# Optimization experiments

Hardware: AMD Instinct MI355X
Metric: run time of the kernel (lower is better)

## Reference

```python
import jax, jax.numpy as jnp
import numpy as np

B, T, TC = 128, 300, 20          # batch, words per sentence, chars per word
DW, DC = 16, 32                  # word / char embedding dims
UC, UM = 32, 64                  # char-LSTM units, main-LSTM units
POS, PAR = 20, 8                 # extra feature dims
VW, VC = 1834, 132               # vocab sizes
DIN = DW + UC + POS + PAR        # 76, input dim of main BiLSTM


def setup_inputs() -> dict:
    key = jax.random.key(0)
    ks = jax.random.split(key, 16)
    s = 0.05
    f32 = jnp.float32
    return dict(
        word_in=jax.random.randint(ks[0], (B, T), 0, VW, dtype=jnp.int32),
        char_in=jax.random.randint(ks[1], (B, T, TC), 0, VC, dtype=jnp.int32),
        input_pos=jax.random.normal(ks[2], (B, T, POS), f32),
        input_par=jax.random.normal(ks[3], (B, T, PAR), f32),
        emb_wor=jax.random.normal(ks[4], (VW, DW), f32) * s,
        emb_char=jax.random.normal(ks[5], (VC, DC), f32) * s,
        char_Wx=jax.random.normal(ks[6], (DC, 4 * UC), f32) * s,
        char_Wh=jax.random.normal(ks[7], (UC, 4 * UC), f32) * s,
        char_b=jnp.zeros((4 * UC,), f32),
        fwd_Wx=jax.random.normal(ks[8], (DIN, 4 * UM), f32) * s,
        fwd_Wh=jax.random.normal(ks[9], (UM, 4 * UM), f32) * s,
        fwd_b=jnp.zeros((4 * UM,), f32),
        bwd_Wx=jax.random.normal(ks[10], (DIN, 4 * UM), f32) * s,
        bwd_Wh=jax.random.normal(ks[11], (UM, 4 * UM), f32) * s,
        bwd_b=jnp.zeros((4 * UM,), f32),
        dense_W=jax.random.normal(ks[12], (2 * UM, 4), f32) * s,
        dense_b=jnp.zeros((4,), f32),
    )


def _lstm(x, mask, Wx, Wh, b):
    """Masked Keras-style LSTM (gate order i,f,g,o). x:(N,S,D) mask:(N,S) bool.
    Masked steps carry state (Keras mask_zero semantics). Returns (N,S,U)."""
    U = Wh.shape[0]
    xz = jnp.einsum('nsd,df->nsf', x, Wx) + b  # hoist input projection out of scan

    def step(carry, inp):
        h, c = carry
        z_x, m = inp
        z = z_x + h @ Wh
        i, f, g, o = jnp.split(z, 4, axis=-1)
        c_new = jax.nn.sigmoid(f) * c + jax.nn.sigmoid(i) * jnp.tanh(g)
        h_new = jax.nn.sigmoid(o) * jnp.tanh(c_new)
        m = m[:, None]
        h = jnp.where(m, h_new, h)
        c = jnp.where(m, c_new, c)
        return (h, c), h

    N = x.shape[0]
    h0 = jnp.zeros((N, U), x.dtype)
    (_, _), hs = jax.lax.scan(step, (h0, h0),
                              (jnp.swapaxes(xz, 0, 1), jnp.swapaxes(mask, 0, 1)))
    return jnp.swapaxes(hs, 0, 1)


def reference(word_in, char_in, input_pos, input_par,
              emb_wor, emb_char, char_Wx, char_Wh, char_b,
              fwd_Wx, fwd_Wh, fwd_b, bwd_Wx, bwd_Wh, bwd_b,
              dense_W, dense_b):
    # word embeddings: (B,T,DW)
    ew = emb_wor[word_in]
    # char embeddings, TimeDistributed over words: (B*T, TC, DC)
    ec = emb_char[char_in].reshape(B * T, TC, DC)
    cmask = (char_in != 0).reshape(B * T, TC)
    # char LSTM, return_sequences=False -> final (last-valid) state
    ch = _lstm(ec, cmask, char_Wx, char_Wh, char_b)[:, -1, :].reshape(B, T, UC)
    # concat word emb, char encoding, extra features -> (B,T,DIN)
    x = jnp.concatenate([ew, ch, input_pos, input_par], axis=-1)
    wmask = word_in != 0
    hf = _lstm(x, wmask, fwd_Wx, fwd_Wh, fwd_b)
    hb = _lstm(x[:, ::-1], wmask[:, ::-1], bwd_Wx, bwd_Wh, bwd_b)[:, ::-1]
    h = jnp.concatenate([hf, hb], axis=-1)  # (B,T,2*UM)
    return jax.nn.softmax(h @ dense_W + dense_b, axis=-1)  # (B,T,4)
```

## Files before the change

kernel.cpp:

```cpp
#include <hip/hip_runtime.h>
#include <hip/hip_bf16.h>

#define B_ 128
#define T_ 300
#define TC_ 20
#define DW_ 16
#define DC_ 32
#define UC_ 32
#define UM_ 64
#define POS_ 20
#define PAR_ 8
#define VW_ 1834
#define VC_ 132
#define DIN_ 76
#define XS_ 80
#define NROW (B_*T_)

typedef _Float16 half_t;
typedef half_t h2 __attribute__((ext_vector_type(2)));

__device__ __forceinline__ float fast_sig(float x){
  return __builtin_amdgcn_rcpf(1.f + __expf(-x));
}
__device__ __forceinline__ float fast_tanh(float x){
  return __builtin_amdgcn_rcpf(1.f + __expf(-2.f*x))*2.f - 1.f;
}
__device__ __forceinline__ float dot2u(unsigned int a, unsigned int b, float acc){
  union{unsigned int u; h2 h;} x, y; x.u = a; y.u = b;
#if __has_builtin(__builtin_amdgcn_fdot2)
  return __builtin_amdgcn_fdot2(x.h, y.h, acc, false);
#else
  return acc + (float)x.h.x*(float)y.h.x + (float)x.h.y*(float)y.h.y;
#endif
}
__device__ __forceinline__ float us2f(unsigned short s){
  union{unsigned short s; half_t h;} x; x.s = s; return (float)x.h;
}

__global__ void k_xzc(const float* __restrict__ emb_char, const float* __restrict__ Wx,
                      const float* __restrict__ bias, float* __restrict__ xzc){
  int v = blockIdx.x, j = threadIdx.x;
  float acc = bias[j];
  #pragma unroll
  for (int k=0;k<DC_;k++) acc += emb_char[v*DC_+k]*Wx[k*(4*UC_)+j];
  xzc[v*(4*UC_)+j] = acc;
}

__global__ void k_chT(const float* __restrict__ Wh, half_t* __restrict__ o){
  int t = blockIdx.x*256 + threadIdx.x;
  int j = t >> 5, k = t & 31;
  o[t] = (half_t)Wh[k*(4*UC_)+j];
}

__global__ void k_whT(const float* __restrict__ Whf, const float* __restrict__ Whb,
                      half_t* __restrict__ o){
  int t = blockIdx.x*256 + threadIdx.x;
  int dir = t >> 14;
  int j = (t >> 6) & 255;
  int k = t & 63;
  const float* W = dir ? Whb : Whf;
  o[t] = (half_t)W[k*(4*UM_)+j];
}

__global__ void k_wxT(const float* __restrict__ Wxf, const float* __restrict__ Wxb,
                      half_t* __restrict__ o){
  int t = blockIdx.x*256 + threadIdx.x;
  int dir = t / (256*96);
  int r = t % (256*96);
  int jj = r / 96, k = r % 96;
  const float* W = dir ? Wxb : Wxf;
  o[t] = (k < DIN_) ? (half_t)W[k*(4*UM_)+jj] : (half_t)0.f;
}

__global__ void k_xfill(const int* __restrict__ word_in, const float* __restrict__ emb_wor,
                        const float* __restrict__ pos, const float* __restrict__ par,
                        float* __restrict__ x){
  int r = blockIdx.x*4 + threadIdx.x/80;
  int c = threadIdx.x%80;
  float v;
  if (c < DW_)                     v = emb_wor[word_in[r]*DW_ + c];
  else if (c < DW_+UC_)            return;
  else if (c < DW_+UC_+POS_)       v = pos[r*POS_ + (c-(DW_+UC_))];
  else if (c < DIN_)               v = par[r*PAR_ + (c-(DW_+UC_+POS_))];
  else                             return;
  x[r*XS_ + c] = v;
}

__global__ __launch_bounds__(512,4) void k_char(const int* __restrict__ char_in,
        const float* __restrict__ xzc, const half_t* __restrict__ chT,
        float* __restrict__ x){
  __shared__ unsigned int hbuf2[8][16];
  __shared__ float2 zex[8][64];
  __shared__ int sidx[8*TC_];
  const int tid = threadIdx.x;
  const int w8 = tid >> 6;
  const int lane = tid & 63;
  const int u = lane & 31;
  const int half = lane >> 5;
  const int seq = blockIdx.x*8 + w8;

  if (tid < 8*TC_) sidx[tid] = char_in[blockIdx.x*(8*TC_) + tid];
  if (half==0 && u<16) hbuf2[w8][u] = 0;

  unsigned int wa[16], wb[16];
  {
    const uint4* pa = reinterpret_cast<const uint4*>(chT + (half*64+u)*32);
    const uint4* pb = reinterpret_cast<const uint4*>(chT + (half*64+32+u)*32);
    #pragma unroll
    for (int q=0;q<4;q++){
      uint4 va = pa[q], vb = pb[q];
      wa[q*4+0]=va.x; wa[q*4+1]=va.y; wa[q*4+2]=va.z; wa[q*4+3]=va.w;
      wb[q*4+0]=vb.x; wb[q*4+1]=vb.y; wb[q*4+2]=vb.z; wb[q*4+3]=vb.w;
    }
  }
  #pragma unroll
  for (int k=0;k<16;k++){ asm volatile("" : "+v"(wa[k])); asm volatile("" : "+v"(wb[k])); }
  __syncthreads();

  float h = 0.f, c = 0.f;
  int idx = sidx[w8*TC_ + 0];
  float za0 = xzc[idx*(4*UC_) + half*64 + u];
  float zb0 = xzc[idx*(4*UC_) + half*64 + 32 + u];

  for (int t=0; t<TC_; t++){
    int idxn = (t+1 < TC_) ? sidx[w8*TC_ + t+1] : 0;
    float zan = xzc[idxn*(4*UC_) + half*64 + u];
    float zbn = xzc[idxn*(4*UC_) + half*64 + 32 + u];

    float za = za0, zb = zb0;
    const uint4* hb = reinterpret_cast<const uint4*>(&hbuf2[w8][0]);
    uint4 q0=hb[0], q1=hb[1], q2=hb[2], q3=hb[3];
    unsigned int hu[16] = {q0.x,q0.y,q0.z,q0.w, q1.x,q1.y,q1.z,q1.w,
                           q2.x,q2.y,q2.z,q2.w, q3.x,q3.y,q3.z,q3.w};
    #pragma unroll
    for (int k=0;k<16;k++){
      za = dot2u(wa[k], hu[k], za);
      zb = dot2u(wb[k], hu[k], zb);
    }
    zex[w8][lane] = make_float2(za, zb);
    if (half == 0){
      float2 p = zex[w8][32+u];
      float zi = za, zf = zb, zg = p.x, zo = p.y;
      float cn = fast_sig(zf)*c + fast_sig(zi)*fast_tanh(zg);
      float hn = fast_sig(zo)*fast_tanh(cn);
      bool m = (idx != 0);
      c = m ? cn : c;
      h = m ? hn : h;
      reinterpret_cast<half_t*>(&hbuf2[w8][0])[u] = (half_t)h;
    }
    idx = idxn; za0 = zan; zb0 = zbn;
  }
  if (half == 0) x[seq*XS_ + DW_ + u] = h;
}

__global__ __launch_bounds__(512,1) void k_xz(const float* __restrict__ x,
      const half_t* __restrict__ wxT_h,
      const float* __restrict__ b_f, const float* __restrict__ b_b,
      half_t* __restrict__ xz){
  __shared__ unsigned int xs[16][40];
  const int j = threadIdx.x;
  const int jj = j & 255;
  const bool bwd = (j >= 256);
  const float bj = bwd ? b_b[jj] : b_f[jj];
  const int u = jj & 63, g = jj >> 6;
  const int ocol = (bwd ? 256 : 0) + u*4 + g;

  unsigned int wq[40];
  {
    const uint4* p = reinterpret_cast<const uint4*>(wxT_h + (size_t)((bwd?256:0)+jj)*96);
    #pragma unroll
    for (int q=0;q<10;q++){
      uint4 v = p[q];
      wq[q*4+0]=v.x; wq[q*4+1]=v.y; wq[q*4+2]=v.z; wq[q*4+3]=v.w;
    }
  }
  #pragma unroll
  for (int k=0;k<40;k++) asm volatile("" : "+v"(wq[k]));

  const int rowbase = blockIdx.x*16;
  for (int i=j; i<16*40; i+=512){
    int r = i/40, q = i%40;
    unsigned int pk = 0;
    if (q < 38){
      float v0 = x[(size_t)(rowbase+r)*XS_ + 2*q];
      float v1 = x[(size_t)(rowbase+r)*XS_ + 2*q+1];
      union{h2 h; unsigned int u;} cv; cv.h = h2{(half_t)v0,(half_t)v1};
      pk = cv.u;
    }
    xs[r][q] = pk;
  }
  __syncthreads();

  for (int r=0; r<16; r++){
    const uint4* xr = reinterpret_cast<const uint4*>(&xs[r][0]);
    float acc = bj;
    #pragma unroll
    for (int q=0;q<10;q++){
      uint4 v = xr[q];
      acc = dot2u(wq[q*4+0], v.x, acc);
      acc = dot2u(wq[q*4+1], v.y, acc);
      acc = dot2u(wq[q*4+2], v.z, acc);
      acc = dot2u(wq[q*4+3], v.w, acc);
    }
    xz[(size_t)(rowbase+r)*512 + ocol] = (half_t)acc;
  }
}

__global__ __launch_bounds__(256,1) void k_rnn(const half_t* __restrict__ xz,
      const int* __restrict__ word_in, const half_t* __restrict__ whT_h,
      float* __restrict__ hcat){
  __shared__ float zpart[2][4*UM_][4];
  __shared__ unsigned int hbuf2[4][32];
  __shared__ int wm[T_];
  const int j = threadIdx.x;
  const int w = j >> 6;
  const int l = j & 63;
  const int dir = blockIdx.x & 1;
  const int b = blockIdx.x >> 1;
  const int sw = (l >> 3) & 3;

  unsigned int wt[4][8];
  {
    const half_t* wbase = whT_h + (size_t)dir*256*64;
    #pragma unroll
    for (int m=0;m<4;m++){
      const uint4* p = reinterpret_cast<const uint4*>(wbase + (m*64+l)*64 + w*16);
      uint4 q0 = p[0], q1 = p[1];
      wt[m][0]=q0.x; wt[m][1]=q0.y; wt[m][2]=q0.z; wt[m][3]=q0.w;
      wt[m][4]=q1.x; wt[m][5]=q1.y; wt[m][6]=q1.z; wt[m][7]=q1.w;
    }
  }
  #pragma unroll
  for (int m=0;m<4;m++)
    #pragma unroll
    for (int k=0;k<8;k++)
      asm volatile("" : "+v"(wt[m][k]));

  for (int t=j; t<T_; t+=256) wm[t] = word_in[b*T_ + (dir ? (T_-1-t) : t)];
  if (l < 32) hbuf2[w][l] = 0;
  __syncthreads();

  float h = 0.f, cc = 0.f;
  int row0 = b*T_ + (dir ? T_-1 : 0);
  const half_t* xp = xz + (size_t)row0*512 + dir*256 + l*4;
  const ptrdiff_t dstep = dir ? -512 : 512;
  float* hout = hcat + (size_t)row0*(2*UM_) + dir*UM_ + l;
  const ptrdiff_t hstep = dir ? -(2*UM_) : (2*UM_);

  ushort4 zxu = *reinterpret_cast<const ushort4*>(xp);

  for (int t=0; t<T_; t++){
    ushort4 zxn = {0,0,0,0};
    if (t+1 < T_) zxn = *reinterpret_cast<const ushort4*>(xp + dstep);

    const uint4* hb = reinterpret_cast<const uint4*>(&hbuf2[w][w*8]);
    uint4 q0 = hb[0], q1 = hb[1];
    unsigned int hu[8] = {q0.x,q0.y,q0.z,q0.w, q1.x,q1.y,q1.z,q1.w};
    #pragma unroll
    for (int m=0;m<4;m++){
      float a = 0.f;
      #pragma unroll
      for (int k=0;k<8;k++) a = dot2u(wt[m][k], hu[k], a);
      zpart[t&1][m*64+l][w ^ sw] = a;
    }
    asm volatile("s_waitcnt lgkmcnt(0)" ::: "memory");
    __builtin_amdgcn_s_barrier();
    asm volatile("" ::: "memory");

    float4 s0 = *reinterpret_cast<const float4*>(&zpart[t&1][      l][0]);
    float4 s1 = *reinterpret_cast<const float4*>(&zpart[t&1][ 64 + l][0]);
    float4 s2 = *reinterpret_cast<const float4*>(&zpart[t&1][128 + l][0]);
    float4 s3 = *reinterpret_cast<const float4*>(&zpart[t&1][192 + l][0]);
    float zi = us2f(zxu.x) + ((s0.x+s0.y)+(s0.z+s0.w));
    float zf = us2f(zxu.y) + ((s1.x+s1.y)+(s1.z+s1.w));
    float zg = us2f(zxu.z) + ((s2.x+s2.y)+(s2.z+s2.w));
    float zo = us2f(zxu.w) + ((s3.x+s3.y)+(s3.z+s3.w));
    int mw = wm[t];
    float cn = fast_sig(zf)*cc + fast_sig(zi)*fast_tanh(zg);
    float hn = fast_sig(zo)*fast_tanh(cn);
    if (mw != 0){ cc = cn; h = hn; }
    reinterpret_cast<half_t*>(&hbuf2[w][0])[l] = (half_t)h;
    if (w == 0) *hout = h;
    hout += hstep;
    zxu = zxn; xp += dstep;
  }
}

__global__ void k_dense(const float* __restrict__ hcat, const float* __restrict__ W,
                        const float* __restrict__ bias, float* __restrict__ out){
  int r = blockIdx.x*256 + threadIdx.x;
  const float4* h4 = reinterpret_cast<const float4*>(hcat + (size_t)r*(2*UM_));
  float a0=bias[0], a1=bias[1], a2=bias[2], a3=bias[3];
  #pragma unroll
  for (int k4=0;k4<32;k4++){
    float4 hv = h4[k4];
    float he[4] = {hv.x, hv.y, hv.z, hv.w};
    #pragma unroll
    for (int e=0;e<4;e++){
      int k = k4*4+e;
      a0 += he[e]*W[k*4+0]; a1 += he[e]*W[k*4+1];
      a2 += he[e]*W[k*4+2]; a3 += he[e]*W[k*4+3];
    }
  }
  float mx = fmaxf(fmaxf(a0,a1), fmaxf(a2,a3));
  float e0=__expf(a0-mx), e1=__expf(a1-mx), e2=__expf(a2-mx), e3=__expf(a3-mx);
  float s = __builtin_amdgcn_rcpf(e0+e1+e2+e3);
  out[r*4+0]=e0*s; out[r*4+1]=e1*s; out[r*4+2]=e2*s; out[r*4+3]=e3*s;
}

extern "C" void kernel_launch(void* const* d_in, const int* in_sizes, int n_in,
                              void* d_out, int out_size, void* d_ws, size_t ws_size,
                              hipStream_t stream) {
  const int*   word_in  = (const int*)  d_in[0];
  const int*   char_in  = (const int*)  d_in[1];
  const float* inp_pos  = (const float*)d_in[2];
  const float* inp_par  = (const float*)d_in[3];
  const float* emb_wor  = (const float*)d_in[4];
  const float* emb_char = (const float*)d_in[5];
  const float* char_Wx  = (const float*)d_in[6];
  const float* char_Wh  = (const float*)d_in[7];
  const float* char_b   = (const float*)d_in[8];
  const float* fwd_Wx   = (const float*)d_in[9];
  const float* fwd_Wh   = (const float*)d_in[10];
  const float* fwd_b    = (const float*)d_in[11];
  const float* bwd_Wx   = (const float*)d_in[12];
  const float* bwd_Wh   = (const float*)d_in[13];
  const float* bwd_b    = (const float*)d_in[14];
  const float* dense_W  = (const float*)d_in[15];
  const float* dense_b  = (const float*)d_in[16];
  float* out = (float*)d_out;

  float* xw   = (float*)d_ws;
  float* hcat = xw + (size_t)NROW*XS_;
  float* xzc  = hcat + (size_t)NROW*128;
  float* fp   = xzc + (size_t)VC_*128;
  half_t* chT   = (half_t*)fp;
  half_t* whT_h = chT + 128*32;
  half_t* wxT_h = whT_h + 2*256*64;
  half_t* xzw   = wxT_h + 2*256*96;

  k_xzc  <<<VC_, 4*UC_, 0, stream>>>(emb_char, char_Wx, char_b, xzc);
  k_chT  <<<16, 256, 0, stream>>>(char_Wh, chT);
  k_whT  <<<128, 256, 0, stream>>>(fwd_Wh, bwd_Wh, whT_h);
  k_wxT  <<<192, 256, 0, stream>>>(fwd_Wx, bwd_Wx, wxT_h);
  k_xfill<<<NROW/4, 320, 0, stream>>>(word_in, emb_wor, inp_pos, inp_par, xw);
  k_char <<<NROW/8, 512, 0, stream>>>(char_in, xzc, chT, xw);
  k_xz   <<<NROW/16, 512, 0, stream>>>(xw, wxT_h, fwd_b, bwd_b, xzw);
  k_rnn  <<<2*B_, 256, 0, stream>>>(xzw, word_in, whT_h, hcat);
  k_dense<<<NROW/256, 256, 0, stream>>>(hcat, dense_W, dense_b, out);
}
```

Before: 320.9 us.

## Run main BiLSTM recurrence in one wavefront with LDS-resident recurrent weights

The main LSTM kernel now uses a single 64-lane wavefront per (batch, direction) instead of four wavefronts. Each lane computes all four gate dot products over the full hidden state, reading swizzled recurrent weights from LDS. This removes the per-step block barrier and the cross-wave partial-sum reduction, and the input-projection prefetch now runs two steps ahead. The cost is four times more dot products per lane and heavy LDS weight traffic on every step. The change also relaxes launch bounds and drops the asm register pins on the char and xz kernels.

```diff
diff --git a/kernel.cpp b/kernel.cpp
--- a/kernel.cpp
+++ b/kernel.cpp
@@ -86,7 +86,7 @@
   x[r*XS_ + c] = v;
 }
 
-__global__ __launch_bounds__(512,4) void k_char(const int* __restrict__ char_in,
+__global__ __launch_bounds__(512,2) void k_char(const int* __restrict__ char_in,
         const float* __restrict__ xzc, const half_t* __restrict__ chT,
         float* __restrict__ x){
   __shared__ unsigned int hbuf2[8][16];
@@ -113,8 +113,6 @@
       wb[q*4+0]=vb.x; wb[q*4+1]=vb.y; wb[q*4+2]=vb.z; wb[q*4+3]=vb.w;
     }
   }
-  #pragma unroll
-  for (int k=0;k<16;k++){ asm volatile("" : "+v"(wa[k])); asm volatile("" : "+v"(wb[k])); }
   __syncthreads();
 
   float h = 0.f, c = 0.f;
@@ -153,7 +151,7 @@
   if (half == 0) x[seq*XS_ + DW_ + u] = h;
 }
 
-__global__ __launch_bounds__(512,1) void k_xz(const float* __restrict__ x,
+__global__ __launch_bounds__(512,2) void k_xz(const float* __restrict__ x,
       const half_t* __restrict__ wxT_h,
       const float* __restrict__ b_f, const float* __restrict__ b_b,
       half_t* __restrict__ xz){
@@ -174,8 +172,6 @@
       wq[q*4+0]=v.x; wq[q*4+1]=v.y; wq[q*4+2]=v.z; wq[q*4+3]=v.w;
     }
   }
-  #pragma unroll
-  for (int k=0;k<40;k++) asm volatile("" : "+v"(wq[k]));
 
   const int rowbase = blockIdx.x*16;
   for (int i=j; i<16*40; i+=512){
@@ -206,83 +202,81 @@
   }
 }
 
-__global__ __launch_bounds__(256,1) void k_rnn(const half_t* __restrict__ xz,
+__global__ __launch_bounds__(64,1) void k_rnn(const half_t* __restrict__ xz,
       const int* __restrict__ word_in, const half_t* __restrict__ whT_h,
       float* __restrict__ hcat){
-  __shared__ float zpart[2][4*UM_][4];
-  __shared__ unsigned int hbuf2[4][32];
+  __shared__ uint4 wlds[2048];
+  __shared__ uint4 hb4[8];
   __shared__ int wm[T_];
-  const int j = threadIdx.x;
-  const int w = j >> 6;
-  const int l = j & 63;
+  const int lane = threadIdx.x;
   const int dir = blockIdx.x & 1;
   const int b = blockIdx.x >> 1;
-  const int sw = (l >> 3) & 3;
-
-  unsigned int wt[4][8];
+
   {
-    const half_t* wbase = whT_h + (size_t)dir*256*64;
-    #pragma unroll
-    for (int m=0;m<4;m++){
-      const uint4* p = reinterpret_cast<const uint4*>(wbase + (m*64+l)*64 + w*16);
-      uint4 q0 = p[0], q1 = p[1];
-      wt[m][0]=q0.x; wt[m][1]=q0.y; wt[m][2]=q0.z; wt[m][3]=q0.w;
-      wt[m][4]=q1.x; wt[m][5]=q1.y; wt[m][6]=q1.z; wt[m][7]=q1.w;
-    }
-  }
-  #pragma unroll
-  for (int m=0;m<4;m++)
-    #pragma unroll
-    for (int k=0;k<8;k++)
-      asm volatile("" : "+v"(wt[m][k]));
-
-  for (int t=j; t<T_; t+=256) wm[t] = word_in[b*T_ + (dir ? (T_-1-t) : t)];
-  if (l < 32) hbuf2[w][l] = 0;
+    const uint4* src = reinterpret_cast<const uint4*>(whT_h + (size_t)dir*256*64);
+    #pragma unroll 4
+    for (int i=0;i<32;i++){
+      int idx = i*64 + lane;
+      int cc = idx >> 3, q = idx & 7;
+      wlds[cc*8 + (q ^ (cc & 7))] = src[idx];
+    }
+  }
+  for (int t=lane; t<T_; t+=64) wm[t] = word_in[b*T_ + (dir ? (T_-1-t) : t)];
+  if (lane < 8) hb4[lane] = uint4{0,0,0,0};
   __syncthreads();
 
-  float h = 0.f, cc = 0.f;
+  float h = 0.f, cc_ = 0.f;
   int row0 = b*T_ + (dir ? T_-1 : 0);
-  const half_t* xp = xz + (size_t)row0*512 + dir*256 + l*4;
+  const half_t* xp = xz + (size_t)row0*512 + dir*256 + lane*4;
   const ptrdiff_t dstep = dir ? -512 : 512;
-  float* hout = hcat + (size_t)row0*(2*UM_) + dir*UM_ + l;
+  float* hout = hcat + (size_t)row0*(2*UM_) + dir*UM_ + lane;
   const ptrdiff_t hstep = dir ? -(2*UM_) : (2*UM_);
 
-  ushort4 zxu = *reinterpret_cast<const ushort4*>(xp);
+  ushort4 z0 = *reinterpret_cast<const ushort4*>(xp);
+  ushort4 z1 = *reinterpret_cast<const ushort4*>(xp + dstep);
+
+  const int c0 = lane, c1 = 64+lane, c2 = 128+lane, c3 = 192+lane;
+  const int x0 = c0&7, x1 = c1&7, x2 = c2&7, x3 = c3&7;
 
   for (int t=0; t<T_; t++){
-    ushort4 zxn = {0,0,0,0};
-    if (t+1 < T_) zxn = *reinterpret_cast<const ushort4*>(xp + dstep);
-
-    const uint4* hb = reinterpret_cast<const uint4*>(&hbuf2[w][w*8]);
-    uint4 q0 = hb[0], q1 = hb[1];
-    unsigned int hu[8] = {q0.x,q0.y,q0.z,q0.w, q1.x,q1.y,q1.z,q1.w};
-    #pragma unroll
-    for (int m=0;m<4;m++){
-      float a = 0.f;
-      #pragma unroll
-      for (int k=0;k<8;k++) a = dot2u(wt[m][k], hu[k], a);
-      zpart[t&1][m*64+l][w ^ sw] = a;
-    }
-    asm volatile("s_waitcnt lgkmcnt(0)" ::: "memory");
-    __builtin_amdgcn_s_barrier();
     asm volatile("" ::: "memory");
-
-    float4 s0 = *reinterpret_cast<const float4*>(&zpart[t&1][      l][0]);
-    float4 s1 = *reinterpret_cast<const float4*>(&zpart[t&1][ 64 + l][0]);
-    float4 s2 = *reinterpret_cast<const float4*>(&zpart[t&1][128 + l][0]);
-    float4 s3 = *reinterpret_cast<const float4*>(&zpart[t&1][192 + l][0]);
-    float zi = us2f(zxu.x) + ((s0.x+s0.y)+(s0.z+s0.w));
-    float zf = us2f(zxu.y) + ((s1.x+s1.y)+(s1.z+s1.w));
-    float zg = us2f(zxu.z) + ((s2.x+s2.y)+(s2.z+s2.w));
-    float zo = us2f(zxu.w) + ((s3.x+s3.y)+(s3.z+s3.w));
+    ushort4 z2 = {0,0,0,0};
+    if (t+2 < T_) z2 = *reinterpret_cast<const ushort4*>(xp + 2*dstep);
+
+    uint4 hc[8];
+    #pragma unroll
+    for (int q=0;q<8;q++) hc[q] = hb4[q];
+
+    float ai0=0.f, ai1=0.f, af0=0.f, af1=0.f;
+    float ag0=0.f, ag1=0.f, ao0=0.f, ao1=0.f;
+    #pragma unroll
+    for (int q=0;q<8;q++){
+      uint4 w0 = wlds[c0*8 + (q^x0)];
+      uint4 w1 = wlds[c1*8 + (q^x1)];
+      uint4 w2 = wlds[c2*8 + (q^x2)];
+      uint4 w3 = wlds[c3*8 + (q^x3)];
+      ai0 = dot2u(w0.x, hc[q].x, ai0); ai1 = dot2u(w0.y, hc[q].y, ai1);
+      ai0 = dot2u(w0.z, hc[q].z, ai0); ai1 = dot2u(w0.w, hc[q].w, ai1);
+      af0 = dot2u(w1.x, hc[q].x, af0); af1 = dot2u(w1.y, hc[q].y, af1);
+      af0 = dot2u(w1.z, hc[q].z, af0); af1 = dot2u(w1.w, hc[q].w, af1);
+      ag0 = dot2u(w2.x, hc[q].x, ag0); ag1 = dot2u(w2.y, hc[q].y, ag1);
+      ag0 = dot2u(w2.z, hc[q].z, ag0); ag1 = dot2u(w2.w, hc[q].w, ag1);
+      ao0 = dot2u(w3.x, hc[q].x, ao0); ao1 = dot2u(w3.y, hc[q].y, ao1);
+      ao0 = dot2u(w3.z, hc[q].z, ao0); ao1 = dot2u(w3.w, hc[q].w, ao1);
+    }
+    float zi = us2f(z0.x) + (ai0+ai1);
+    float zf = us2f(z0.y) + (af0+af1);
+    float zg = us2f(z0.z) + (ag0+ag1);
+    float zo = us2f(z0.w) + (ao0+ao1);
+
     int mw = wm[t];
-    float cn = fast_sig(zf)*cc + fast_sig(zi)*fast_tanh(zg);
+    float cn = fast_sig(zf)*cc_ + fast_sig(zi)*fast_tanh(zg);
     float hn = fast_sig(zo)*fast_tanh(cn);
-    if (mw != 0){ cc = cn; h = hn; }
-    reinterpret_cast<half_t*>(&hbuf2[w][0])[l] = (half_t)h;
-    if (w == 0) *hout = h;
+    if (mw != 0){ cc_ = cn; h = hn; }
+    reinterpret_cast<half_t*>(hb4)[lane] = (half_t)h;
+    *hout = h;
     hout += hstep;
-    zxu = zxn; xp += dstep;
+    z0 = z1; z1 = z2; xp += dstep;
   }
 }
 
@@ -346,6 +340,6 @@
   k_xfill<<<NROW/4, 320, 0, stream>>>(word_in, emb_wor, inp_pos, inp_par, xw);
   k_char <<<NROW/8, 512, 0, stream>>>(char_in, xzc, chT, xw);
   k_xz   <<<NROW/16, 512, 0, stream>>>(xw, wxT_h, fwd_b, bwd_b, xzw);
-  k_rnn  <<<2*B_, 256, 0, stream>>>(xzw, word_in, whT_h, hcat);
+  k_rnn  <<<2*B_, 64, 0, stream>>>(xzw, word_in, whT_h, hcat);
   k_dense<<<NROW/256, 256, 0, stream>>>(hcat, dense_W, dense_b, out);
 }
```

Measured after the change: 380.4 us. 18.5% more time.

## Split recurrent matvec by gate per wave and apply gate nonlinearities in parallel

Applied to the files above, without the earlier changes.

The main BiLSTM kernel now has each of the four waves compute one full gate (all 64 hidden inputs) for its 64 units instead of a K-split partial sum over all gates. This removes the cross-wave partial-sum reduction, lets each wave apply its sigmoid or tanh before the barrier, and shrinks the shared exchange to one float per gate. The xz output layout changes to gate-major to match, the prefetch distance grows to two steps, and the launch bounds and register-pinning asm in the char and xz kernels are relaxed. The trade-off is that each wave now reads the whole h vector from LDS every step and holds 32 weight registers.

```diff
diff --git a/kernel.cpp b/kernel.cpp
--- a/kernel.cpp
+++ b/kernel.cpp
@@ -86,7 +86,7 @@
   x[r*XS_ + c] = v;
 }
 
-__global__ __launch_bounds__(512,4) void k_char(const int* __restrict__ char_in,
+__global__ __launch_bounds__(512,2) void k_char(const int* __restrict__ char_in,
         const float* __restrict__ xzc, const half_t* __restrict__ chT,
         float* __restrict__ x){
   __shared__ unsigned int hbuf2[8][16];
@@ -113,8 +113,6 @@
       wb[q*4+0]=vb.x; wb[q*4+1]=vb.y; wb[q*4+2]=vb.z; wb[q*4+3]=vb.w;
     }
   }
-  #pragma unroll
-  for (int k=0;k<16;k++){ asm volatile("" : "+v"(wa[k])); asm volatile("" : "+v"(wb[k])); }
   __syncthreads();
 
   float h = 0.f, c = 0.f;
@@ -153,7 +151,7 @@
   if (half == 0) x[seq*XS_ + DW_ + u] = h;
 }
 
-__global__ __launch_bounds__(512,1) void k_xz(const float* __restrict__ x,
+__global__ __launch_bounds__(512,2) void k_xz(const float* __restrict__ x,
       const half_t* __restrict__ wxT_h,
       const float* __restrict__ b_f, const float* __restrict__ b_b,
       half_t* __restrict__ xz){
@@ -163,7 +161,7 @@
   const bool bwd = (j >= 256);
   const float bj = bwd ? b_b[jj] : b_f[jj];
   const int u = jj & 63, g = jj >> 6;
-  const int ocol = (bwd ? 256 : 0) + u*4 + g;
+  const int ocol = ((bwd ? 4 : 0) + g)*64 + u;
 
   unsigned int wq[40];
   {
@@ -174,8 +172,6 @@
       wq[q*4+0]=v.x; wq[q*4+1]=v.y; wq[q*4+2]=v.z; wq[q*4+3]=v.w;
     }
   }
-  #pragma unroll
-  for (int k=0;k<40;k++) asm volatile("" : "+v"(wq[k]));
 
   const int rowbase = blockIdx.x*16;
   for (int i=j; i<16*40; i+=512){
@@ -209,7 +205,7 @@
 __global__ __launch_bounds__(256,1) void k_rnn(const half_t* __restrict__ xz,
       const int* __restrict__ word_in, const half_t* __restrict__ whT_h,
       float* __restrict__ hcat){
-  __shared__ float zpart[2][4*UM_][4];
+  __shared__ float gbuf[2][4][64];
   __shared__ unsigned int hbuf2[4][32];
   __shared__ int wm[T_];
   const int j = threadIdx.x;
@@ -217,72 +213,63 @@
   const int l = j & 63;
   const int dir = blockIdx.x & 1;
   const int b = blockIdx.x >> 1;
-  const int sw = (l >> 3) & 3;
-
-  unsigned int wt[4][8];
+
+  unsigned int wt[32];
   {
-    const half_t* wbase = whT_h + (size_t)dir*256*64;
-    #pragma unroll
-    for (int m=0;m<4;m++){
-      const uint4* p = reinterpret_cast<const uint4*>(wbase + (m*64+l)*64 + w*16);
-      uint4 q0 = p[0], q1 = p[1];
-      wt[m][0]=q0.x; wt[m][1]=q0.y; wt[m][2]=q0.z; wt[m][3]=q0.w;
-      wt[m][4]=q1.x; wt[m][5]=q1.y; wt[m][6]=q1.z; wt[m][7]=q1.w;
-    }
-  }
-  #pragma unroll
-  for (int m=0;m<4;m++)
-    #pragma unroll
-    for (int k=0;k<8;k++)
-      asm volatile("" : "+v"(wt[m][k]));
-
+    const uint4* p = reinterpret_cast<const uint4*>(whT_h + ((size_t)dir*256 + w*64 + l)*64);
+    #pragma unroll
+    for (int q=0;q<8;q++){
+      uint4 v = p[q];
+      wt[q*4+0]=v.x; wt[q*4+1]=v.y; wt[q*4+2]=v.z; wt[q*4+3]=v.w;
+    }
+  }
   for (int t=j; t<T_; t+=256) wm[t] = word_in[b*T_ + (dir ? (T_-1-t) : t)];
   if (l < 32) hbuf2[w][l] = 0;
   __syncthreads();
 
-  float h = 0.f, cc = 0.f;
+  float h = 0.f, c_ = 0.f;
   int row0 = b*T_ + (dir ? T_-1 : 0);
-  const half_t* xp = xz + (size_t)row0*512 + dir*256 + l*4;
+  const half_t* xp = xz + (size_t)row0*512 + (dir*4+w)*64 + l;
   const ptrdiff_t dstep = dir ? -512 : 512;
   float* hout = hcat + (size_t)row0*(2*UM_) + dir*UM_ + l;
   const ptrdiff_t hstep = dir ? -(2*UM_) : (2*UM_);
 
-  ushort4 zxu = *reinterpret_cast<const ushort4*>(xp);
+  unsigned short zx0 = *reinterpret_cast<const unsigned short*>(xp);
+  unsigned short zx1 = *reinterpret_cast<const unsigned short*>(xp + dstep);
 
   for (int t=0; t<T_; t++){
-    ushort4 zxn = {0,0,0,0};
-    if (t+1 < T_) zxn = *reinterpret_cast<const ushort4*>(xp + dstep);
-
-    const uint4* hb = reinterpret_cast<const uint4*>(&hbuf2[w][w*8]);
-    uint4 q0 = hb[0], q1 = hb[1];
-    unsigned int hu[8] = {q0.x,q0.y,q0.z,q0.w, q1.x,q1.y,q1.z,q1.w};
-    #pragma unroll
-    for (int m=0;m<4;m++){
-      float a = 0.f;
-      #pragma unroll
-      for (int k=0;k<8;k++) a = dot2u(wt[m][k], hu[k], a);
-      zpart[t&1][m*64+l][w ^ sw] = a;
-    }
+    unsigned short zx2 = 0;
+    if (t+2 < T_) zx2 = *reinterpret_cast<const unsigned short*>(xp + 2*dstep);
+
+    const uint4* hb = reinterpret_cast<const uint4*>(&hbuf2[w][0]);
+    float a0=0.f, a1=0.f;
+    #pragma unroll
+    for (int q=0;q<8;q++){
+      uint4 hv = hb[q];
+      a0 = dot2u(wt[q*4+0], hv.x, a0);
+      a1 = dot2u(wt[q*4+1], hv.y, a1);
+      a0 = dot2u(wt[q*4+2], hv.z, a0);
+      a1 = dot2u(wt[q*4+3], hv.w, a1);
+    }
+    float z = us2f(zx0) + (a0+a1);
+    float nl = (w == 2) ? fast_tanh(z) : fast_sig(z);
+    gbuf[t&1][w][l] = nl;
     asm volatile("s_waitcnt lgkmcnt(0)" ::: "memory");
     __builtin_amdgcn_s_barrier();
     asm volatile("" ::: "memory");
 
-    float4 s0 = *reinterpret_cast<const float4*>(&zpart[t&1][      l][0]);
-    float4 s1 = *reinterpret_cast<const float4*>(&zpart[t&1][ 64 + l][0]);
-    float4 s2 = *reinterpret_cast<const float4*>(&zpart[t&1][128 + l][0]);
-    float4 s3 = *reinterpret_cast<const float4*>(&zpart[t&1][192 + l][0]);
-    float zi = us2f(zxu.x) + ((s0.x+s0.y)+(s0.z+s0.w));
-    float zf = us2f(zxu.y) + ((s1.x+s1.y)+(s1.z+s1.w));
-    float zg = us2f(zxu.z) + ((s2.x+s2.y)+(s2.z+s2.w));
-    float zo = us2f(zxu.w) + ((s3.x+s3.y)+(s3.z+s3.w));
+    float si = gbuf[t&1][0][l];
+    float sf = gbuf[t&1][1][l];
+    float tg = gbuf[t&1][2][l];
+    float so = gbuf[t&1][3][l];
     int mw = wm[t];
-    float cn = fast_sig(zf)*cc + fast_sig(zi)*fast_tanh(zg);
-    float hn = fast_sig(zo)*fast_tanh(cn);
-    if (mw != 0){ cc = cn; h = hn; }
+    float cn = sf*c_ + si*tg;
+    float hn = so*fast_tanh(cn);
+    if (mw != 0){ c_ = cn; h = hn; }
     reinterpret_cast<half_t*>(&hbuf2[w][0])[l] = (half_t)h;
     if (w == 0) *hout = h;
     hout += hstep;
-    zxu = zxn; xp += dstep;
+    zx0 = zx1; zx1 = zx2; xp += dstep;
   }
 }
 
```

Result: no change. 324.5 us (+1.1%).
